# Kernel optimization log

Measured on AMD Instinct MI355X. Metric: run time of the kernel, lower is better.

## Reference

```python
import jax, jax.numpy as jnp
import numpy as np

N, E, D, H = 50000, 800000, 128, 4

def setup_inputs() -> dict:
    key = jax.random.key(0)
    ks = jax.random.split(key, 6)
    x = jax.random.normal(ks[0], (N, D), dtype=jnp.float32)
    edge_index = jax.random.randint(ks[1], (2, E), 0, N, dtype=jnp.int64)
    W = jax.random.normal(ks[2], (D, H * D), dtype=jnp.float32) * (1.0 / np.sqrt(D))
    att_src = jax.random.normal(ks[3], (H, D), dtype=jnp.float32) * 0.1
    att_dst = jax.random.normal(ks[4], (H, D), dtype=jnp.float32) * 0.1
    bias = jnp.zeros((D,), dtype=jnp.float32)
    gamma = jnp.ones((D,), dtype=jnp.float32)
    beta = jnp.zeros((D,), dtype=jnp.float32)
    return {"x": x, "edge_index": edge_index, "W": W, "att_src": att_src,
            "att_dst": att_dst, "bias": bias, "gamma": gamma, "beta": beta}

def reference(x, edge_index, W, att_src, att_dst, bias, gamma, beta):
    src, dst = edge_index[0], edge_index[1]
    # GATConv: linear transform per head -> [N, H, D]
    xw = (x @ W).reshape(N, H, D)
    a_src = jnp.einsum('nhd,hd->nh', xw, att_src)  # [N, H]
    a_dst = jnp.einsum('nhd,hd->nh', xw, att_dst)  # [N, H]
    alpha = a_src[src] + a_dst[dst]                # [E, H]
    alpha = jax.nn.leaky_relu(alpha, negative_slope=0.2)
    # segment softmax over incoming edges of each dst node
    m = jax.ops.segment_max(alpha, dst, num_segments=N)   # [N, H]
    ex = jnp.exp(alpha - m[dst])                            # [E, H]
    denom = jax.ops.segment_sum(ex, dst, num_segments=N)   # [N, H]
    attn = ex / denom[dst]                                  # [E, H]
    msg = xw[src] * attn[:, :, None]                        # [E, H, D]
    agg = jax.ops.segment_sum(msg, dst, num_segments=N)    # [N, H, D]
    out = agg.mean(axis=1) + bias                           # concat=False: mean heads
    # LayerNorm (eps=1e-5)
    mu = out.mean(axis=-1, keepdims=True)
    var = out.var(axis=-1, keepdims=True)
    out = (out - mu) * jax.lax.rsqrt(var + 1e-5) * gamma + beta
    out = jax.nn.gelu(out, approximate=False)
    return out + x  # project is Identity (in_channels == out_channels)
```

## Files before the change

### kernel.cpp

```cpp
#include <hip/hip_runtime.h>
#include <hip/hip_bf16.h>
#include <hip/hip_fp16.h>
#include <math.h>

#define ND 128
#define NH 4
#define HD 512

typedef __attribute__((ext_vector_type(8))) short bf16x8;
typedef __attribute__((ext_vector_type(4))) float f32x4;
typedef __attribute__((ext_vector_type(2))) float f32x2;

__device__ __forceinline__ unsigned pack_bf16(float a, float b) {
    unsigned ua = __float_as_uint(a), ub = __float_as_uint(b);
    ua = (ua + 0x7fffu + ((ua >> 16) & 1u)) >> 16;
    ub = (ub + 0x7fffu + ((ub >> 16) & 1u)) >> 16;
    return ua | (ub << 16);
}
__device__ __forceinline__ unsigned short bf16r(float a) {
    unsigned ua = __float_as_uint(a);
    return (unsigned short)((ua + 0x7fffu + ((ua >> 16) & 1u)) >> 16);
}
__device__ __forceinline__ float bflo(unsigned u) { return __uint_as_float(u << 16); }
__device__ __forceinline__ float bfhi(unsigned u) { return __uint_as_float(u & 0xffff0000u); }
__device__ __forceinline__ unsigned pack_half2(float a, float b) {
    __half ha = __float2half(a), hb = __float2half(b);
    return (unsigned)__half_as_ushort(ha) | ((unsigned)__half_as_ushort(hb) << 16);
}
__device__ __forceinline__ float2 h22f(unsigned u) {
    __half2 h = *(__half2*)&u;
    return __half22float2(h);
}

__global__ __launch_bounds__(256) void prep_misc(const float* __restrict__ W,
                                                 const float* __restrict__ att_src,
                                                 const float* __restrict__ att_dst,
                                                 unsigned short* __restrict__ Ws,
                                                 float* __restrict__ pt,
                                                 const int* __restrict__ dst,
                                                 int* __restrict__ cnt, int ne) {
    int b = blockIdx.x;
    if (b < 16) {
        __shared__ float tile[64][65];
        int h = b >> 2, rt = (b >> 1) & 1, ct = b & 1;
        int tx = threadIdx.x;
        int rr = tx >> 6, c = tx & 63;
#pragma unroll
        for (int i = 0; i < 16; ++i) {
            int r = i * 4 + rr;
            tile[r][c] = W[(size_t)(rt * 64 + r) * HD + h * ND + ct * 64 + c];
        }
        __syncthreads();
#pragma unroll
        for (int i = 0; i < 16; ++i) {
            int r = i * 4 + rr;
            Ws[(size_t)(ct * 64 + r) * HD + h * ND + rt * 64 + c] = bf16r(tile[c][r]);
        }
    } else if (b < 48) {
        int w = threadIdx.x >> 6, lane = threadIdx.x & 63;
        int k = (b - 16) * 4 + w;
#pragma unroll
        for (int h = 0; h < NH; ++h) {
            float2 wv = ((const float2*)(W + (size_t)k * HD + h * ND))[lane];
            float2 as = ((const float2*)(att_src + h * ND))[lane];
            float2 ad = ((const float2*)(att_dst + h * ND))[lane];
            float ps = wv.x * as.x + wv.y * as.y;
            float pd = wv.x * ad.x + wv.y * ad.y;
#pragma unroll
            for (int off = 1; off < 64; off <<= 1) {
                ps += __shfl_xor(ps, off);
                pd += __shfl_xor(pd, off);
            }
            if (lane == 0) {
                pt[h * ND + k] = ps;
                pt[(4 + h) * ND + k] = pd;
            }
        }
    } else {
        int e = (b - 48) * 256 + threadIdx.x;
        if (e < ne) atomicAdd(&cnt[dst[e]], 1);
    }
}

__global__ __launch_bounds__(256) void ka_scanA(const float* __restrict__ x,
                                                const float* __restrict__ pt,
                                                unsigned* __restrict__ xb,
                                                float* __restrict__ a_src,
                                                float* __restrict__ a_dst,
                                                const int* __restrict__ cnt,
                                                int* __restrict__ partial,
                                                int* __restrict__ bsum,
                                                int n, int nbA) {
    __shared__ float pl[8 * ND];
    __shared__ int sh[256];
    if ((int)blockIdx.x < nbA) {
        { int t = threadIdx.x; ((float4*)pl)[t] = ((const float4*)pt)[t]; }
        __syncthreads();
        int wave = (blockIdx.x * 256 + threadIdx.x) >> 6;
        int lane = threadIdx.x & 63;
        if (wave >= n) return;
        float2 xv = ((const float2*)(x + (size_t)wave * ND))[lane];
        xb[(size_t)wave * 64 + lane] = pack_bf16(xv.x, xv.y);
#pragma unroll
        for (int o = 0; o < 8; ++o) {
            float2 pv = ((const float2*)(pl + o * ND))[lane];
            float v = xv.x * pv.x + xv.y * pv.y;
#pragma unroll
            for (int off = 1; off < 64; off <<= 1) v += __shfl_xor(v, off);
            if (lane == 0) {
                if (o < 4) a_src[(size_t)wave * NH + o] = v;
                else       a_dst[(size_t)wave * NH + (o - 4)] = v;
            }
        }
    } else {
        int bid = blockIdx.x - nbA;
        int gid = bid * 256 + threadIdx.x;
        int v = (gid < n) ? cnt[gid] : 0;
        int val = v;
        sh[threadIdx.x] = val;
        __syncthreads();
#pragma unroll
        for (int off = 1; off < 256; off <<= 1) {
            int add = (threadIdx.x >= off) ? sh[threadIdx.x - off] : 0;
            __syncthreads();
            val += add;
            sh[threadIdx.x] = val;
            __syncthreads();
        }
        if (gid < n) partial[gid] = val - v;
        if (threadIdx.x == 255) bsum[bid] = val;
    }
}

__global__ __launch_bounds__(256) void scanBC(const int* __restrict__ partial,
                                              const int* __restrict__ bsum,
                                              int* __restrict__ starts,
                                              int* __restrict__ cursor,
                                              int n, int ne, int nb) {
    __shared__ int sh[256];
    int t = threadIdx.x;
    int v = (t < nb) ? bsum[t] : 0;
    int val = v;
    sh[t] = val;
    __syncthreads();
#pragma unroll
    for (int off = 1; off < 256; off <<= 1) {
        int add = (t >= off) ? sh[t - off] : 0;
        __syncthreads();
        val += add;
        sh[t] = val;
        __syncthreads();
    }
    int myoff = (blockIdx.x == 0) ? 0 : sh[blockIdx.x - 1];
    int gid = blockIdx.x * 256 + t;
    if (gid < n) {
        int s = partial[gid] + myoff;
        starts[gid] = s;
        cursor[gid] = s;
    }
    if (gid == 0) starts[n] = ne;
}

__global__ __launch_bounds__(256) void scatter_edges_w(const int* __restrict__ src,
                                                       const int* __restrict__ dst,
                                                       const float* __restrict__ a_src,
                                                       const float* __restrict__ a_dst,
                                                       int* __restrict__ cursor,
                                                       uint4* __restrict__ eperm, int ne) {
    int e = blockIdx.x * 256 + threadIdx.x;
    if (e < ne) {
        int s = src[e], t = dst[e];
        float4 as = *(const float4*)(a_src + (size_t)s * NH);
        float4 ad = *(const float4*)(a_dst + (size_t)t * NH);
        float A0 = as.x + ad.x, A1 = as.y + ad.y, A2 = as.z + ad.z, A3 = as.w + ad.w;
        A0 = (A0 > 0.f) ? A0 : 0.2f * A0;
        A1 = (A1 > 0.f) ? A1 : 0.2f * A1;
        A2 = (A2 > 0.f) ? A2 : 0.2f * A2;
        A3 = (A3 > 0.f) ? A3 : 0.2f * A3;
        float e0 = __expf(A0), e1 = __expf(A1), e2 = __expf(A2), e3 = __expf(A3);
        int pos = atomicAdd(&cursor[t], 1);
        uint4 ev;
        ev.x = (unsigned)s;
        ev.y = pack_half2(e0, e1);
        ev.z = pack_half2(e2, e3);
        ev.w = 0u;
        eperm[pos] = ev;
    }
}

#define PK8()                                                              \
    { f32x2 xlo = {bflo(xv.x), bfhi(xv.x)};                                \
      f32x2 xhi = {bflo(xv.y), bfhi(xv.y)};                                \
      acc2[0] += xlo * w01.x; acc2[1] += xhi * w01.x;                      \
      acc2[2] += xlo * w01.y; acc2[3] += xhi * w01.y;                      \
      acc2[4] += xlo * w23.x; acc2[5] += xhi * w23.x;                      \
      acc2[6] += xlo * w23.y; acc2[7] += xhi * w23.y; }

__global__ __launch_bounds__(256) void node_agg(const uint4* __restrict__ eperm,
                                                const int* __restrict__ starts,
                                                const uint2* __restrict__ xb2,
                                                unsigned* __restrict__ u, int n) {
    __shared__ uint4 estage[4][16];
    const int w = threadIdx.x >> 6;
    int node = blockIdx.x * 4 + w;
    int lane = threadIdx.x & 63;
    if (node >= n) return;
    const int slot = lane & 31;
    const int half = lane >> 5;

    int s0 = starts[node], s1 = starts[node + 1];

    float den0 = 0.f, den1 = 0.f, den2 = 0.f, den3 = 0.f;
    f32x2 acc2[8];
#pragma unroll
    for (int j = 0; j < 8; ++j) acc2[j] = (f32x2){0.f, 0.f};

    for (int base = s0; base < s1; base += 16) {
        int rem = s1 - base; if (rem > 16) rem = 16;
        uint4 ev = {0u, 0u, 0u, 0u};
        if (lane < rem) ev = eperm[base + lane];
        if (lane < 16) estage[w][lane] = ev;
        {
            float2 dl = h22f(ev.y), dh = h22f(ev.z);
            den0 += dl.x; den1 += dl.y; den2 += dh.x; den3 += dh.y;
        }
#pragma unroll
        for (int pp = 0; pp < 8; ++pp) {
            uint4 e2 = estage[w][2 * pp + half];
            uint2 xv = xb2[(size_t)e2.x * 32 + slot];
            float2 w01 = h22f(e2.y), w23 = h22f(e2.z);
            PK8();
        }
    }

#pragma unroll
    for (int off = 1; off < 64; off <<= 1) {
        den0 += __shfl_xor(den0, off);
        den1 += __shfl_xor(den1, off);
        den2 += __shfl_xor(den2, off);
        den3 += __shfl_xor(den3, off);
    }
    float i0 = (den0 > 0.f) ? 0.25f / den0 : 0.f;
    float i1 = (den1 > 0.f) ? 0.25f / den1 : 0.f;
    float i2 = (den2 > 0.f) ? 0.25f / den2 : 0.f;
    float i3 = (den3 > 0.f) ? 0.25f / den3 : 0.f;

    float v[16];
#pragma unroll
    for (int hh4 = 0; hh4 < 4; ++hh4) {
        float ih = (hh4 == 0) ? i0 : (hh4 == 1) ? i1 : (hh4 == 2) ? i2 : i3;
        v[hh4 * 4 + 0] = acc2[hh4 * 2].x * ih;
        v[hh4 * 4 + 1] = acc2[hh4 * 2].y * ih;
        v[hh4 * 4 + 2] = acc2[hh4 * 2 + 1].x * ih;
        v[hh4 * 4 + 3] = acc2[hh4 * 2 + 1].y * ih;
    }
#pragma unroll
    for (int j = 0; j < 16; ++j) v[j] += __shfl_xor(v[j], 32);

#pragma unroll
    for (int hh = 0; hh < 2; ++hh) {
        int h = half * 2 + hh;
        uint2 val;
        val.x = pack_bf16(v[h * 4 + 0], v[h * 4 + 1]);
        val.y = pack_bf16(v[h * 4 + 2], v[h * 4 + 3]);
        ((uint2*)u)[(size_t)node * 128 + h * 32 + slot] = val;
    }
}

__global__ __launch_bounds__(256) void gemm_out(
        const unsigned short* __restrict__ u, const unsigned short* __restrict__ Ws,
        const float* __restrict__ x, const float* __restrict__ bias,
        const float* __restrict__ gamma, const float* __restrict__ beta,
        float* __restrict__ out, int n) {
    __shared__ char Bs[32768];
    const int t = threadIdx.x;
    const int w = t >> 6, l = t & 63;
    const int e16 = l & 15, g16 = l >> 4;
    const int row0 = blockIdx.x * 64;

    int ar = row0 + w * 16 + e16; if (ar >= n) ar = n - 1;
    const unsigned short* ap = u + (size_t)ar * HD + g16 * 8;

    f32x4 acc[8];
#pragma unroll
    for (int nr = 0; nr < 8; ++nr) acc[nr] = (f32x4){0.f, 0.f, 0.f, 0.f};

    const int swz = (e16 & 7) << 4;
    for (int kc = 0; kc < 4; ++kc) {
        if (kc) __syncthreads();
#pragma unroll
        for (int i = 0; i < 8; ++i) {
            int c = t + i * 256;
            int nl = c >> 4, kb = c & 15;
            uint4 pv = *(const uint4*)(Ws + (size_t)nl * HD + kc * 128 + kb * 8);
            *(uint4*)(Bs + nl * 256 + ((kb * 16) ^ ((nl & 7) << 4))) = pv;
        }
        __syncthreads();

#pragma unroll
        for (int ks = 0; ks < 4; ++ks) {
            int koff = (ks * 64 + g16 * 16) ^ swz;
            bf16x8 a0 = *(const bf16x8*)(ap + kc * 128 + ks * 32);
#pragma unroll
            for (int nr = 0; nr < 8; ++nr) {
                bf16x8 b = *(const bf16x8*)(Bs + (nr * 16 + e16) * 256 + koff);
                acc[nr] = __builtin_amdgcn_mfma_f32_16x16x32_bf16(a0, b, acc[nr], 0, 0, 0);
            }
        }
    }

    float bias_l[8], gam_l[8], bet_l[8];
#pragma unroll
    for (int c = 0; c < 8; ++c) {
        bias_l[c] = bias[c * 16 + e16];
        gam_l[c]  = gamma[c * 16 + e16];
        bet_l[c]  = beta[c * 16 + e16];
    }
#pragma unroll
    for (int ri = 0; ri < 4; ++ri) {
        int grow = row0 + w * 16 + g16 * 4 + ri;
        float val[8];
        float s = 0.f, s2 = 0.f;
#pragma unroll
        for (int c = 0; c < 8; ++c) {
            val[c] = acc[c][ri] + bias_l[c];
            s += val[c]; s2 += val[c] * val[c];
        }
#pragma unroll
        for (int off = 1; off < 16; off <<= 1) {
            s += __shfl_xor(s, off);
            s2 += __shfl_xor(s2, off);
        }
        float mu = s * (1.0f / ND);
        float var = fmaxf(s2 * (1.0f / ND) - mu * mu, 0.0f);
        float inv = rsqrtf(var + 1e-5f);
        if (grow < n) {
#pragma unroll
            for (int c = 0; c < 8; ++c) {
                float y = (val[c] - mu) * inv * gam_l[c] + bet_l[c];
                y = 0.5f * y * (1.0f + erff(y * 0.70710678118654752f));
                out[(size_t)grow * ND + c * 16 + e16] =
                    y + x[(size_t)grow * ND + c * 16 + e16];
            }
        }
    }
}

extern "C" void kernel_launch(void* const* d_in, const int* in_sizes, int n_in,
                              void* d_out, int out_size, void* d_ws, size_t ws_size,
                              hipStream_t stream) {
    const float* x       = (const float*)d_in[0];
    const int*   edge    = (const int*)d_in[1];
    const float* W       = (const float*)d_in[2];
    const float* att_src = (const float*)d_in[3];
    const float* att_dst = (const float*)d_in[4];
    const float* bias    = (const float*)d_in[5];
    const float* gamma   = (const float*)d_in[6];
    const float* beta    = (const float*)d_in[7];
    float* out = (float*)d_out;

    const int n  = in_sizes[0] / ND;
    const int ne = in_sizes[1] / 2;
    const int* src = edge;
    const int* dst = edge + ne;

    const int nb  = (n + 255) / 256;
    const int nbA = (n + 3) / 4;

    char* wsp = (char*)d_ws;
    unsigned* xb        = (unsigned*)wsp;        wsp += (size_t)n * 64 * sizeof(unsigned);
    unsigned short* u   = (unsigned short*)wsp;  wsp += (size_t)n * HD * sizeof(short);
    unsigned short* Ws  = (unsigned short*)wsp;  wsp += (size_t)ND * HD * sizeof(short);
    float* pt      = (float*)wsp;               wsp += (size_t)8 * ND * sizeof(float);
    float* a_src   = (float*)wsp;               wsp += (size_t)n * NH * sizeof(float);
    float* a_dst   = (float*)wsp;               wsp += (size_t)n * NH * sizeof(float);
    uint4* eperm   = (uint4*)wsp;               wsp += (size_t)ne * sizeof(uint4);
    int*   cnt     = (int*)wsp;                 wsp += (size_t)n * sizeof(int);
    int*   partial = (int*)wsp;                 wsp += (size_t)n * sizeof(int);
    int*   bsum    = (int*)wsp;                 wsp += 256 * sizeof(int);
    int*   starts  = (int*)wsp;                 wsp += (size_t)(n + 1) * sizeof(int);
    int*   cursor  = (int*)wsp;                 wsp += (size_t)n * sizeof(int);

    (void)hipMemsetAsync(cnt, 0, (size_t)n * sizeof(int), stream);

    prep_misc<<<48 + (ne + 255) / 256, 256, 0, stream>>>(W, att_src, att_dst,
                                                         Ws, pt, dst, cnt, ne);

    ka_scanA<<<nbA + nb, 256, 0, stream>>>(x, pt, xb, a_src, a_dst,
                                           cnt, partial, bsum, n, nbA);

    scanBC<<<nb, 256, 0, stream>>>(partial, bsum, starts, cursor, n, ne, nb);

    scatter_edges_w<<<(ne + 255) / 256, 256, 0, stream>>>(src, dst, a_src, a_dst,
                                                          cursor, eperm, ne);

    node_agg<<<(n + 3) / 4, 256, 0, stream>>>(eperm, starts, (const uint2*)xb,
                                              (unsigned*)u, n);

    gemm_out<<<(n + 63) / 64, 256, 0, stream>>>(u, Ws, x, bias, gamma, beta, out, n);
}
```

Baseline: 209.6 us.

## Move attention logit computation into node aggregation and scatter only source ids

The edge scatter kernel now writes only the 4-byte source index per edge instead of a 16-byte record holding packed exp weights. The node aggregation kernel loads a_dst once per node and computes each edge's leaky-relu and exp weights from gathered a_src. This shrinks the permuted edge array and drops the per-edge a_dst gather. In exchange, the random a_src gather and the exp math move into the aggregation kernel's critical path, and the denominator reduction is narrowed to the 16 active lanes plus a broadcast.

```diff
diff --git a/kernel.cpp b/kernel.cpp
--- a/kernel.cpp
+++ b/kernel.cpp
@@ -161,30 +161,14 @@
     if (gid == 0) starts[n] = ne;
 }
 
-__global__ __launch_bounds__(256) void scatter_edges_w(const int* __restrict__ src,
-                                                       const int* __restrict__ dst,
-                                                       const float* __restrict__ a_src,
-                                                       const float* __restrict__ a_dst,
-                                                       int* __restrict__ cursor,
-                                                       uint4* __restrict__ eperm, int ne) {
+__global__ __launch_bounds__(256) void scatter_edges(const int* __restrict__ src,
+                                                     const int* __restrict__ dst,
+                                                     int* __restrict__ cursor,
+                                                     int* __restrict__ srcperm, int ne) {
     int e = blockIdx.x * 256 + threadIdx.x;
     if (e < ne) {
-        int s = src[e], t = dst[e];
-        float4 as = *(const float4*)(a_src + (size_t)s * NH);
-        float4 ad = *(const float4*)(a_dst + (size_t)t * NH);
-        float A0 = as.x + ad.x, A1 = as.y + ad.y, A2 = as.z + ad.z, A3 = as.w + ad.w;
-        A0 = (A0 > 0.f) ? A0 : 0.2f * A0;
-        A1 = (A1 > 0.f) ? A1 : 0.2f * A1;
-        A2 = (A2 > 0.f) ? A2 : 0.2f * A2;
-        A3 = (A3 > 0.f) ? A3 : 0.2f * A3;
-        float e0 = __expf(A0), e1 = __expf(A1), e2 = __expf(A2), e3 = __expf(A3);
-        int pos = atomicAdd(&cursor[t], 1);
-        uint4 ev;
-        ev.x = (unsigned)s;
-        ev.y = pack_half2(e0, e1);
-        ev.z = pack_half2(e2, e3);
-        ev.w = 0u;
-        eperm[pos] = ev;
+        int pos = atomicAdd(&cursor[dst[e]], 1);
+        srcperm[pos] = src[e];
     }
 }
 
@@ -196,8 +180,10 @@
       acc2[4] += xlo * w23.x; acc2[5] += xhi * w23.x;                      \
       acc2[6] += xlo * w23.y; acc2[7] += xhi * w23.y; }
 
-__global__ __launch_bounds__(256) void node_agg(const uint4* __restrict__ eperm,
+__global__ __launch_bounds__(256) void node_agg(const int* __restrict__ srcperm,
                                                 const int* __restrict__ starts,
+                                                const float4* __restrict__ a_src4,
+                                                const float4* __restrict__ a_dst4,
                                                 const uint2* __restrict__ xb2,
                                                 unsigned* __restrict__ u, int n) {
     __shared__ uint4 estage[4][16];
@@ -209,6 +195,7 @@
     const int half = lane >> 5;
 
     int s0 = starts[node], s1 = starts[node + 1];
+    float4 ad = a_dst4[node];
 
     float den0 = 0.f, den1 = 0.f, den2 = 0.f, den3 = 0.f;
     f32x2 acc2[8];
@@ -217,29 +204,46 @@
 
     for (int base = s0; base < s1; base += 16) {
         int rem = s1 - base; if (rem > 16) rem = 16;
-        uint4 ev = {0u, 0u, 0u, 0u};
-        if (lane < rem) ev = eperm[base + lane];
-        if (lane < 16) estage[w][lane] = ev;
-        {
-            float2 dl = h22f(ev.y), dh = h22f(ev.z);
-            den0 += dl.x; den1 += dl.y; den2 += dh.x; den3 += dh.y;
+        int sl = 0; unsigned wy = 0u, wz = 0u;
+        if (lane < rem) {
+            sl = srcperm[base + lane];
+            float4 as = a_src4[sl];
+            float A0 = as.x + ad.x, A1 = as.y + ad.y;
+            float A2 = as.z + ad.z, A3 = as.w + ad.w;
+            A0 = (A0 > 0.f) ? A0 : 0.2f * A0;
+            A1 = (A1 > 0.f) ? A1 : 0.2f * A1;
+            A2 = (A2 > 0.f) ? A2 : 0.2f * A2;
+            A3 = (A3 > 0.f) ? A3 : 0.2f * A3;
+            float e0 = __expf(A0), e1 = __expf(A1);
+            float e2 = __expf(A2), e3 = __expf(A3);
+            den0 += e0; den1 += e1; den2 += e2; den3 += e3;
+            wy = pack_half2(e0, e1);
+            wz = pack_half2(e2, e3);
+        }
+        if (lane < 16) {
+            uint4 ev; ev.x = (unsigned)sl; ev.y = wy; ev.z = wz; ev.w = 0u;
+            estage[w][lane] = ev;
         }
 #pragma unroll
         for (int pp = 0; pp < 8; ++pp) {
-            uint4 e2 = estage[w][2 * pp + half];
-            uint2 xv = xb2[(size_t)e2.x * 32 + slot];
-            float2 w01 = h22f(e2.y), w23 = h22f(e2.z);
+            uint4 e2v = estage[w][2 * pp + half];
+            uint2 xv = xb2[(e2v.x << 5) + (unsigned)slot];
+            float2 w01 = h22f(e2v.y), w23 = h22f(e2v.z);
             PK8();
         }
     }
 
 #pragma unroll
-    for (int off = 1; off < 64; off <<= 1) {
+    for (int off = 1; off < 16; off <<= 1) {
         den0 += __shfl_xor(den0, off);
         den1 += __shfl_xor(den1, off);
         den2 += __shfl_xor(den2, off);
         den3 += __shfl_xor(den3, off);
     }
+    den0 = __shfl(den0, lane & 15);
+    den1 = __shfl(den1, lane & 15);
+    den2 = __shfl(den2, lane & 15);
+    den3 = __shfl(den3, lane & 15);
     float i0 = (den0 > 0.f) ? 0.25f / den0 : 0.f;
     float i1 = (den1 > 0.f) ? 0.25f / den1 : 0.f;
     float i2 = (den2 > 0.f) ? 0.25f / den2 : 0.f;
@@ -374,7 +378,7 @@
     float* pt      = (float*)wsp;               wsp += (size_t)8 * ND * sizeof(float);
     float* a_src   = (float*)wsp;               wsp += (size_t)n * NH * sizeof(float);
     float* a_dst   = (float*)wsp;               wsp += (size_t)n * NH * sizeof(float);
-    uint4* eperm   = (uint4*)wsp;               wsp += (size_t)ne * sizeof(uint4);
+    int*   srcperm = (int*)wsp;                 wsp += (size_t)ne * sizeof(int);
     int*   cnt     = (int*)wsp;                 wsp += (size_t)n * sizeof(int);
     int*   partial = (int*)wsp;                 wsp += (size_t)n * sizeof(int);
     int*   bsum    = (int*)wsp;                 wsp += 256 * sizeof(int);
@@ -391,11 +395,12 @@
 
     scanBC<<<nb, 256, 0, stream>>>(partial, bsum, starts, cursor, n, ne, nb);
 
-    scatter_edges_w<<<(ne + 255) / 256, 256, 0, stream>>>(src, dst, a_src, a_dst,
-                                                          cursor, eperm, ne);
-
-    node_agg<<<(n + 3) / 4, 256, 0, stream>>>(eperm, starts, (const uint2*)xb,
-                                              (unsigned*)u, n);
+    scatter_edges<<<(ne + 255) / 256, 256, 0, stream>>>(src, dst, cursor, srcperm, ne);
+
+    node_agg<<<(n + 3) / 4, 256, 0, stream>>>(srcperm, starts,
+                                              (const float4*)a_src,
+                                              (const float4*)a_dst,
+                                              (const uint2*)xb, (unsigned*)u, n);
 
     gemm_out<<<(n + 63) / 64, 256, 0, stream>>>(u, Ws, x, bias, gamma, beta, out, n);
 }
```

Result: slower. 216.3 us (+3.2%).
